# Performance work log

Measured on AMD Instinct MI355X. Metric: run time of the kernel, lower is better.

The kernel has to match this reference:

```python
import jax, jax.numpy as jnp
import numpy as np

D_MODEL = 256
POOL = 10  # Keras MaxPooling1D(pool_size=10) -> stride 10, padding 'same'


def setup_inputs() -> dict:
    key = jax.random.key(0)
    ks = jax.random.split(key, 11)
    B, S, D = 4, 4096, D_MODEL
    scale = 1.0 / np.sqrt(D)
    inp = {
        "v": jax.random.normal(ks[0], (B, S, D), jnp.float32),
        "k": jax.random.normal(ks[1], (B, S, D), jnp.float32),
        "q": jax.random.normal(ks[2], (B, S, D), jnp.float32),
        "wq": jax.random.normal(ks[3], (D, D), jnp.float32) * scale,
        "bq": jnp.zeros((D,), jnp.float32),
        "wk": jax.random.normal(ks[4], (D, D), jnp.float32) * scale,
        "bk": jnp.zeros((D,), jnp.float32),
        "wv": jax.random.normal(ks[5], (D, D), jnp.float32) * scale,
        "bv": jnp.zeros((D,), jnp.float32),
        "wo": jax.random.normal(ks[6], (D, D), jnp.float32) * scale,
        "bo": jnp.zeros((D,), jnp.float32),
    }
    return inp


def reference(v, k, q, wq, bq, wk, bk, wv, bv, wo, bo):
    d = q.shape[-1]
    qp = q @ wq + bq          # [B,Sq,D]
    kp = k @ wk + bk          # [B,Sk,D]
    vp = v @ wv + bv          # [B,Sk,D]
    scores = jnp.einsum('bqd,bkd->bqk', qp, kp) / jnp.sqrt(jnp.float32(d))
    # MaxPooling1D over the steps (Sq) axis, stride = pool_size, 'same' padding
    pooled = jax.lax.reduce_window(
        scores, -jnp.inf, jax.lax.max,
        window_dimensions=(1, POOL, 1),
        window_strides=(1, POOL, 1),
        padding='SAME')          # [B, ceil(Sq/10), Sk]
    attn = jax.nn.softmax(pooled, axis=-1)
    out = jnp.einsum('bqk,bkd->bqd', attn, vp)
    return out @ wo + bo
```

## Files before the change

### kernel.cpp

```cpp
#include <hip/hip_runtime.h>
#include <hip/hip_bf16.h>
#include <stdint.h>

typedef __attribute__((ext_vector_type(8))) short          bf16x8;
typedef __attribute__((ext_vector_type(4))) float          f32x4;
typedef __attribute__((ext_vector_type(4))) float          f4;
typedef __attribute__((ext_vector_type(8))) unsigned short u16x8;
typedef __attribute__((ext_vector_type(4))) unsigned short u16x4;

#define DEVINL __device__ __forceinline__

static constexpr int B  = 4;
static constexpr int S  = 4096;
static constexpr int D  = 256;
static constexpr int SP = 410;
static constexpr int KZ = 16;
static constexpr int MO = B * SP;
static constexpr size_t PSLICE = (size_t)MO * D;

DEVINL unsigned short f2bf(float x) {
  union { float f; unsigned u; } v; v.f = x;
  unsigned r = v.u + 0x7FFFu + ((v.u >> 16) & 1u);
  return (unsigned short)(r >> 16);
}

DEVINL f32x4 mfma16(bf16x8 a, bf16x8 b, f32x4 c) {
  return __builtin_amdgcn_mfma_f32_16x16x32_bf16(a, b, c, 0, 0, 0);
}

typedef const __attribute__((address_space(1))) void* gas_t;
typedef __attribute__((address_space(3))) void*       las_t;
DEVINL void gload16(const void* g, void* l) {
  __builtin_amdgcn_global_load_lds((gas_t)g, (las_t)l, 16, 0, 0);
}

DEVINL void cfence() { asm volatile("" ::: "memory"); }
DEVINL void barrier_mem() { cfence(); __builtin_amdgcn_s_barrier(); cfence(); }
DEVINL void lds_barrier() {
  asm volatile("s_waitcnt lgkmcnt(0)" ::: "memory");
  __builtin_amdgcn_s_barrier();
  cfence();
}
#define WAIT_VM(N) asm volatile("s_waitcnt vmcnt(" #N ")" ::: "memory")

__global__ __launch_bounds__(256) void cvtwt_kernel(
    const float* __restrict__ xq, const float* __restrict__ xk, const float* __restrict__ xv,
    const float* __restrict__ wq, const float* __restrict__ wk,
    const float* __restrict__ wv, const float* __restrict__ wo,
    unsigned short* __restrict__ oq, unsigned short* __restrict__ ok, unsigned short* __restrict__ ov,
    unsigned short* __restrict__ wt)
{
  int z = blockIdx.y;
  if (z == 3) {
    if (blockIdx.x >= 1024) return;
    int idx = blockIdx.x * 256 + threadIdx.x;
    int mat = idx >> 16;
    int r   = idx & 65535;
    int n   = r >> 8;
    int k   = r & 255;
    const float* w = (mat == 0) ? wq : (mat == 1) ? wk : (mat == 2) ? wv : wo;
    wt[idx] = f2bf(w[k * 256 + n]);
    return;
  }
  const float* x    = (z == 0) ? xq : (z == 1) ? xk : xv;
  unsigned short* o = (z == 0) ? oq : (z == 1) ? ok : ov;
  size_t i = ((size_t)blockIdx.x * 256 + threadIdx.x) * 8;
  f4 a = *reinterpret_cast<const f4*>(x + i);
  f4 c = *reinterpret_cast<const f4*>(x + i + 4);
  u16x8 h;
  h[0] = f2bf(a[0]); h[1] = f2bf(a[1]); h[2] = f2bf(a[2]); h[3] = f2bf(a[3]);
  h[4] = f2bf(c[0]); h[5] = f2bf(c[1]); h[6] = f2bf(c[2]); h[7] = f2bf(c[3]);
  *reinterpret_cast<u16x8*>(o + i) = h;
}

__global__ __launch_bounds__(512) void proj_kernel(
    const unsigned short* __restrict__ xq, const unsigned short* __restrict__ xk,
    const unsigned short* __restrict__ xv, const unsigned short* __restrict__ wt,
    const float* __restrict__ bq, const float* __restrict__ bk, const float* __restrict__ bv,
    unsigned short* __restrict__ qp, unsigned short* __restrict__ kp, unsigned short* __restrict__ vpT)
{
  int z = blockIdx.z;
  const unsigned short* X = (z == 0) ? xq : (z == 1) ? xk : xv;
  const unsigned short* W = wt + z * 65536;
  const float* bias       = (z == 0) ? bq : (z == 1) ? bk : bv;

  int m0 = blockIdx.x * 256;
  int n0 = blockIdx.y * 128;

  __shared__ __align__(16) struct { char A[2][32768]; char Bm[2][16384]; } sm;

  const char* Xc = (const char*)X;
  const char* Wc = (const char*)W;

  int tid  = threadIdx.x;
  int lane = tid & 63, wid = tid >> 6;
  int wr = wid >> 1, wc = wid & 1;
  int lrow = lane & 15, kseg = lane >> 4;

  f32x4 zero4 = {0.f, 0.f, 0.f, 0.f};
  f32x4 acc[4][4];
#pragma unroll
  for (int i = 0; i < 4; i++)
#pragma unroll
    for (int j = 0; j < 4; j++) acc[i][j] = zero4;

  auto stage = [&](int t, int buf) {
#pragma unroll
    for (int i = 0; i < 4; ++i) {
      int inst = wid * 4 + i;
      int sg   = inst * 64 + lane;
      int row  = sg >> 3, c16 = sg & 7;
      gload16(Xc + ((size_t)(m0 + row) << 9) + (t << 7) + ((c16 ^ (row & 7)) << 4),
              sm.A[buf] + inst * 1024);
    }
#pragma unroll
    for (int i = 0; i < 2; ++i) {
      int inst = wid * 2 + i;
      int sg   = inst * 64 + lane;
      int row  = sg >> 3, c16 = sg & 7;
      gload16(Wc + ((size_t)(n0 + row) << 9) + (t << 7) + ((c16 ^ (row & 7)) << 4),
              sm.Bm[buf] + inst * 1024);
    }
  };

  stage(0, 0);
#pragma unroll
  for (int t = 0; t < 4; ++t) {
    int cur = t & 1;
    if (t < 3) { stage(t + 1, cur ^ 1); WAIT_VM(6); } else { WAIT_VM(0); }
    barrier_mem();
    const char* Asm = sm.A[cur];
    const char* Bsm = sm.Bm[cur];
#pragma unroll
    for (int kk = 0; kk < 2; ++kk) {
      bf16x8 af[4], bfr[4];
#pragma unroll
      for (int mi = 0; mi < 4; ++mi) {
        int R = wr * 64 + mi * 16 + lrow;
        int c16 = (kk * 4 + kseg) ^ (R & 7);
        af[mi] = *reinterpret_cast<const bf16x8*>(Asm + R * 128 + c16 * 16);
      }
#pragma unroll
      for (int cf = 0; cf < 4; ++cf) {
        int nl = wc * 64 + cf * 16 + lrow;
        int c16 = (kk * 4 + kseg) ^ (nl & 7);
        bfr[cf] = *reinterpret_cast<const bf16x8*>(Bsm + nl * 128 + c16 * 16);
      }
#pragma unroll
      for (int mi = 0; mi < 4; ++mi)
#pragma unroll
        for (int cf = 0; cf < 4; ++cf)
          acc[mi][cf] = mfma16(af[mi], bfr[cf], acc[mi][cf]);
    }
    barrier_mem();
  }

  int r4 = kseg * 4;
  if (z < 2) {
    unsigned short* Out = (z == 0) ? qp : kp;
#pragma unroll
    for (int mi = 0; mi < 4; mi++)
#pragma unroll
      for (int cf = 0; cf < 4; cf++) {
        int n = n0 + wc * 64 + cf * 16 + lrow;
        float bv_ = bias[n];
#pragma unroll
        for (int r = 0; r < 4; r++) {
          int m = m0 + wr * 64 + mi * 16 + r4 + r;
          Out[(size_t)m * 256 + n] = f2bf(acc[mi][cf][r] + bv_);
        }
      }
  } else {
#pragma unroll
    for (int mi = 0; mi < 4; mi++)
#pragma unroll
      for (int cf = 0; cf < 4; cf++) {
        int n = n0 + wc * 64 + cf * 16 + lrow;
        float bv_ = bias[n];
        u16x4 hh;
#pragma unroll
        for (int r = 0; r < 4; r++) hh[r] = f2bf(acc[mi][cf][r] + bv_);
        int m  = m0 + wr * 64 + mi * 16 + r4;
        int bb = m >> 12, s = m & 4095;
        *reinterpret_cast<u16x4*>(&vpT[(size_t)bb * (256 * 4096) + (size_t)n * 4096 + s]) = hh;
      }
  }
}

__global__ __launch_bounds__(512) void scores_pool_kernel(
    const unsigned short* __restrict__ qp, const unsigned short* __restrict__ kp,
    float* __restrict__ pooled)
{
  int id   = blockIdx.x;
  int nb   = id & 31;
  int b    = (id >> 5) & 3;
  int half = id >> 7;
  int wb0  = half ? 9 : 0;
  int nwb  = half ? 8 : 9;
  int n0   = nb * 128;

  __shared__ __align__(16) struct { char A[2][32768]; char Bm[65536]; } sm;
  float* pm = (float*)sm.A[1];

  const char* qpc = (const char*)(qp + (size_t)b * S * 256);
  const char* kpc = (const char*)(kp + (size_t)b * S * 256);

  int tid  = threadIdx.x;
  int lane = tid & 63, wid = tid >> 6;
  int wr = wid >> 1, wc = wid & 1;
  int lrow = lane & 15, kseg = lane >> 4;
  int h = kseg;

#pragma unroll
  for (int i = 0; i < 8; ++i) {
    int inst = wid * 8 + i;
    int sg   = inst * 64 + lane;
    int row  = sg >> 5, c16 = sg & 31;
    gload16(kpc + ((size_t)(n0 + row) << 9) + (((size_t)(c16 ^ (row & 7))) << 4),
            sm.Bm + inst * 1024);
  }

  auto stageA = [&](int qbt, int ks, int buf) {
#pragma unroll
    for (int i = 0; i < 4; ++i) {
      int inst = wid * 4 + i;
      int sg   = inst * 64 + lane;
      int row  = sg >> 3, c16 = sg & 7;
      int q = qbt + row; q = (q < 0) ? 0 : ((q > S - 1) ? (S - 1) : q);
      gload16(qpc + ((size_t)q << 9) + (ks << 7) + ((c16 ^ (row & 7)) << 4),
              sm.A[buf] + inst * 1024);
    }
  };

  stageA(wb0 * 250 - 2, 0, 0);

  int gmax = nwb * 4;
  for (int i = 0; i < nwb; ++i) {
    int wb = wb0 + i, w0 = wb * 25;
    int qb = w0 * 10 - 2;
    int nwin = SP - w0; if (nwin > 25) nwin = 25;

    f32x4 zero4 = {0.f, 0.f, 0.f, 0.f};
    f32x4 acc[4][4];
#pragma unroll
    for (int mi = 0; mi < 4; mi++)
#pragma unroll
      for (int cf = 0; cf < 4; cf++) acc[mi][cf] = zero4;

#pragma unroll
    for (int ks = 0; ks < 4; ++ks) {
      int g  = (i << 2) | ks;
      int gn = g + 1;
      if (gn < gmax) {
        int i2 = gn >> 2, ks2 = gn & 3;
        stageA((wb0 + i2) * 250 - 2, ks2, gn & 1);
        WAIT_VM(4);
      } else {
        WAIT_VM(0);
      }
      barrier_mem();
      const char* Asm = sm.A[g & 1];
#pragma unroll
      for (int kk = 0; kk < 2; ++kk) {
        bf16x8 af[4], bfr[4];
#pragma unroll
        for (int mi = 0; mi < 4; ++mi) {
          int R = wr * 64 + mi * 16 + lrow;
          int c16 = (kk * 4 + kseg) ^ (R & 7);
          af[mi] = *reinterpret_cast<const bf16x8*>(Asm + R * 128 + c16 * 16);
        }
#pragma unroll
        for (int cf = 0; cf < 4; ++cf) {
          int nl = wc * 64 + cf * 16 + lrow;
          int c16 = ((ks << 3) + kk * 4 + kseg) ^ (nl & 7);
          bfr[cf] = *reinterpret_cast<const bf16x8*>(sm.Bm + nl * 512 + c16 * 16);
        }
#pragma unroll
        for (int mi = 0; mi < 4; ++mi)
#pragma unroll
          for (int cf = 0; cf < 4; ++cf)
            acc[mi][cf] = mfma16(af[mi], bfr[cf], acc[mi][cf]);
      }
      barrier_mem();
    }

#pragma unroll
    for (int c = 0; c < 2; ++c) {
      if (wc == c) {
#pragma unroll
        for (int mi = 0; mi < 4; ++mi) {
          int p = wr * 32 + mi * 8 + h * 2;
#pragma unroll
          for (int cf = 0; cf < 4; ++cf) {
            int col = cf * 16 + lrow;
            pm[p * 64 + col]       = fmaxf(acc[mi][cf][0], acc[mi][cf][1]);
            pm[(p + 1) * 64 + col] = fmaxf(acc[mi][cf][2], acc[mi][cf][3]);
          }
        }
      }
      lds_barrier();
      for (int s = tid; s < 1600; s += 512) {
        int j = s >> 6, col = s & 63;
        if (j < nwin) {
          float m = -3.4e38f;
#pragma unroll
          for (int t5 = 0; t5 < 5; ++t5) {
            int p  = 5 * j + t5;
            int q0 = qb + 2 * p;
            if (q0 >= 0 && q0 < S) m = fmaxf(m, pm[p * 64 + col]);
          }
          pooled[((size_t)b * SP + w0 + j) * 4096 + n0 + c * 64 + col] = m * 0.0625f;
        }
      }
      lds_barrier();
    }
  }
}

__global__ __launch_bounds__(256) void softmax_kernel(
    const float* __restrict__ pooled, unsigned short* __restrict__ attn)
{
  int row = blockIdx.x;
  const float* p = pooled + (size_t)row * 4096;
  unsigned short* a = attn + (size_t)row * 4096;
  int tid = threadIdx.x;
  int lane = tid & 63, wid = tid >> 6;

  f4 v[4];
  float mx = -3.4e38f;
#pragma unroll
  for (int i = 0; i < 4; i++) {
    v[i] = *reinterpret_cast<const f4*>(&p[i * 1024 + tid * 4]);
    mx = fmaxf(mx, fmaxf(fmaxf(v[i][0], v[i][1]), fmaxf(v[i][2], v[i][3])));
  }
#pragma unroll
  for (int off = 32; off > 0; off >>= 1) mx = fmaxf(mx, __shfl_xor(mx, off, 64));
  __shared__ float redm[4];
  __shared__ float reds[4];
  if (lane == 0) redm[wid] = mx;
  __syncthreads();
  mx = fmaxf(fmaxf(redm[0], redm[1]), fmaxf(redm[2], redm[3]));

  float e[16];
  float sum = 0.f;
#pragma unroll
  for (int i = 0; i < 4; i++)
#pragma unroll
    for (int j = 0; j < 4; j++) {
      float t = __expf(v[i][j] - mx);
      e[i * 4 + j] = t;
      sum += t;
    }
#pragma unroll
  for (int off = 32; off > 0; off >>= 1) sum += __shfl_xor(sum, off, 64);
  if (lane == 0) reds[wid] = sum;
  __syncthreads();
  sum = reds[0] + reds[1] + reds[2] + reds[3];
  float inv = 1.f / sum;
#pragma unroll
  for (int i = 0; i < 4; i++) {
    u16x4 o;
#pragma unroll
    for (int j = 0; j < 4; j++) o[j] = f2bf(e[i * 4 + j] * inv);
    *reinterpret_cast<u16x4*>(&a[i * 1024 + tid * 4]) = o;
  }
}

__global__ __launch_bounds__(256) void pv_kernel(
    const unsigned short* __restrict__ attn, const unsigned short* __restrict__ vpT,
    float* __restrict__ part)
{
  int bx = blockIdx.x;
  int b  = bx >> 2, mt = bx & 3;
  int m0 = mt * 128;
  int n0 = blockIdx.y * 128;
  int kz = blockIdx.z;
  int k0b = kz * 512;

  const char* Ac = (const char*)(attn + (size_t)b * SP * 4096);
  const char* Bc = (const char*)(vpT  + (size_t)b * 256 * 4096);
  float* Pz = part + (size_t)kz * PSLICE;

  __shared__ __align__(16) struct { char A[2][16384]; char Bm[2][16384]; } sm;

  int tid  = threadIdx.x;
  int lane = tid & 63, wid = tid >> 6;
  int wr = wid >> 1, wc = wid & 1;
  int lrow = lane & 15, kseg = lane >> 4;

  f32x4 zero4 = {0.f, 0.f, 0.f, 0.f};
  f32x4 acc[4][4];
#pragma unroll
  for (int i = 0; i < 4; i++)
#pragma unroll
    for (int j = 0; j < 4; j++) acc[i][j] = zero4;

  auto stage = [&](int t, int buf) {
#pragma unroll
    for (int i = 0; i < 4; ++i) {
      int inst = wid * 4 + i;
      int sg   = inst * 64 + lane;
      int row  = sg >> 3, c16 = sg & 7;
      int m = m0 + row; m = (m > SP - 1) ? (SP - 1) : m;
      gload16(Ac + (size_t)m * 8192 + k0b + (t << 7) + ((c16 ^ (row & 7)) << 4),
              sm.A[buf] + inst * 1024);
    }
#pragma unroll
    for (int i = 0; i < 4; ++i) {
      int inst = wid * 4 + i;
      int sg   = inst * 64 + lane;
      int row  = sg >> 3, c16 = sg & 7;
      gload16(Bc + (size_t)(n0 + row) * 8192 + k0b + (t << 7) + ((c16 ^ (row & 7)) << 4),
              sm.Bm[buf] + inst * 1024);
    }
  };

  stage(0, 0);
#pragma unroll
  for (int t = 0; t < 4; ++t) {
    int cur = t & 1;
    if (t < 3) { stage(t + 1, cur ^ 1); WAIT_VM(8); } else { WAIT_VM(0); }
    barrier_mem();
    const char* Asm = sm.A[cur];
    const char* Bsm = sm.Bm[cur];
#pragma unroll
    for (int kk = 0; kk < 2; ++kk) {
      bf16x8 af[4], bfr[4];
#pragma unroll
      for (int mi = 0; mi < 4; ++mi) {
        int R = wr * 64 + mi * 16 + lrow;
        int c16 = (kk * 4 + kseg) ^ (R & 7);
        af[mi] = *reinterpret_cast<const bf16x8*>(Asm + R * 128 + c16 * 16);
      }
#pragma unroll
      for (int cf = 0; cf < 4; ++cf) {
        int nl = wc * 64 + cf * 16 + lrow;
        int c16 = (kk * 4 + kseg) ^ (nl & 7);
        bfr[cf] = *reinterpret_cast<const bf16x8*>(Bsm + nl * 128 + c16 * 16);
      }
#pragma unroll
      for (int mi = 0; mi < 4; ++mi)
#pragma unroll
        for (int cf = 0; cf < 4; ++cf)
          acc[mi][cf] = mfma16(af[mi], bfr[cf], acc[mi][cf]);
    }
    barrier_mem();
  }

  int r4 = kseg * 4;
#pragma unroll
  for (int mi = 0; mi < 4; mi++)
#pragma unroll
    for (int cf = 0; cf < 4; cf++) {
      int n = n0 + wc * 64 + cf * 16 + lrow;
#pragma unroll
      for (int r = 0; r < 4; r++) {
        int m = m0 + wr * 64 + mi * 16 + r4 + r;
        if (m < SP) Pz[((size_t)b * SP + m) * 256 + n] = acc[mi][cf][r];
      }
    }
}

__global__ __launch_bounds__(256) void reduce_kernel(
    const float* __restrict__ part, unsigned short* __restrict__ ctxb)
{
  size_t i = (size_t)blockIdx.x * 256 + threadIdx.x;
  float s = 0.f;
#pragma unroll
  for (int z = 0; z < KZ; ++z) s += part[z * PSLICE + i];
  ctxb[i] = f2bf(s);
}

__global__ __launch_bounds__(512) void out_kernel(
    const unsigned short* __restrict__ ctxb, const unsigned short* __restrict__ woT,
    const float* __restrict__ bo, float* __restrict__ out)
{
  int m0 = blockIdx.x * 256;
  int n0 = blockIdx.y * 128;

  __shared__ __align__(16) struct { char A[2][32768]; char Bm[2][16384]; } sm;

  const char* Xc = (const char*)ctxb;
  const char* Wc = (const char*)woT;

  int tid  = threadIdx.x;
  int lane = tid & 63, wid = tid >> 6;
  int wr = wid >> 1, wc = wid & 1;
  int lrow = lane & 15, kseg = lane >> 4;

  f32x4 zero4 = {0.f, 0.f, 0.f, 0.f};
  f32x4 acc[4][4];
#pragma unroll
  for (int i = 0; i < 4; i++)
#pragma unroll
    for (int j = 0; j < 4; j++) acc[i][j] = zero4;

  auto stage = [&](int t, int buf) {
#pragma unroll
    for (int i = 0; i < 4; ++i) {
      int inst = wid * 4 + i;
      int sg   = inst * 64 + lane;
      int row  = sg >> 3, c16 = sg & 7;
      int m = m0 + row; m = (m > MO - 1) ? (MO - 1) : m;
      gload16(Xc + ((size_t)m << 9) + (t << 7) + ((c16 ^ (row & 7)) << 4),
              sm.A[buf] + inst * 1024);
    }
#pragma unroll
    for (int i = 0; i < 2; ++i) {
      int inst = wid * 2 + i;
      int sg   = inst * 64 + lane;
      int row  = sg >> 3, c16 = sg & 7;
      gload16(Wc + ((size_t)(n0 + row) << 9) + (t << 7) + ((c16 ^ (row & 7)) << 4),
              sm.Bm[buf] + inst * 1024);
    }
  };

  stage(0, 0);
#pragma unroll
  for (int t = 0; t < 4; ++t) {
    int cur = t & 1;
    if (t < 3) { stage(t + 1, cur ^ 1); WAIT_VM(6); } else { WAIT_VM(0); }
    barrier_mem();
    const char* Asm = sm.A[cur];
    const char* Bsm = sm.Bm[cur];
#pragma unroll
    for (int kk = 0; kk < 2; ++kk) {
      bf16x8 af[4], bfr[4];
#pragma unroll
      for (int mi = 0; mi < 4; ++mi) {
        int R = wr * 64 + mi * 16 + lrow;
        int c16 = (kk * 4 + kseg) ^ (R & 7);
        af[mi] = *reinterpret_cast<const bf16x8*>(Asm + R * 128 + c16 * 16);
      }
#pragma unroll
      for (int cf = 0; cf < 4; ++cf) {
        int nl = wc * 64 + cf * 16 + lrow;
        int c16 = (kk * 4 + kseg) ^ (nl & 7);
        bfr[cf] = *reinterpret_cast<const bf16x8*>(Bsm + nl * 128 + c16 * 16);
      }
#pragma unroll
      for (int mi = 0; mi < 4; ++mi)
#pragma unroll
        for (int cf = 0; cf < 4; ++cf)
          acc[mi][cf] = mfma16(af[mi], bfr[cf], acc[mi][cf]);
    }
    barrier_mem();
  }

  int r4 = kseg * 4;
#pragma unroll
  for (int mi = 0; mi < 4; mi++)
#pragma unroll
    for (int cf = 0; cf < 4; cf++) {
      int n = n0 + wc * 64 + cf * 16 + lrow;
      float bv_ = bo[n];
#pragma unroll
      for (int r = 0; r < 4; r++) {
        int m = m0 + wr * 64 + mi * 16 + r4 + r;
        if (m < MO) out[(size_t)m * 256 + n] = acc[mi][cf][r] + bv_;
      }
    }
}

extern "C" void kernel_launch(void* const* d_in, const int* in_sizes, int n_in,
                              void* d_out, int out_size, void* d_ws, size_t ws_size,
                              hipStream_t stream)
{
  const float* v  = (const float*)d_in[0];
  const float* k  = (const float*)d_in[1];
  const float* q  = (const float*)d_in[2];
  const float* wq = (const float*)d_in[3];
  const float* bq = (const float*)d_in[4];
  const float* wk = (const float*)d_in[5];
  const float* bk = (const float*)d_in[6];
  const float* wv = (const float*)d_in[7];
  const float* bv = (const float*)d_in[8];
  const float* wo = (const float*)d_in[9];
  const float* bo = (const float*)d_in[10];
  float* out = (float*)d_out;

  char* ws = (char*)d_ws;
  size_t off = 0;
  auto alloc = [&](size_t bytes) -> void* {
    void* p = ws + off;
    off += (bytes + 255) & ~(size_t)255;
    return p;
  };
  unsigned short* qp   = (unsigned short*)alloc((size_t)B * S * D * 2);
  unsigned short* kp   = (unsigned short*)alloc((size_t)B * S * D * 2);
  unsigned short* vpT  = (unsigned short*)alloc((size_t)B * S * D * 2);
  unsigned short* wt   = (unsigned short*)alloc((size_t)4 * 256 * 256 * 2);
  unsigned short* ctxb = (unsigned short*)alloc(PSLICE * 2);
  char* shared_region  = (char*)alloc((size_t)B * SP * 4096 * 4);
  unsigned short* attn = (unsigned short*)alloc((size_t)B * SP * 4096 * 2);

  unsigned short* qx = (unsigned short*)shared_region;
  unsigned short* kx = qx + (size_t)B * S * D;
  unsigned short* vx = kx + (size_t)B * S * D;
  float* pooled = (float*)shared_region;
  float* part   = (float*)shared_region;

  cvtwt_kernel<<<dim3(2048, 4), 256, 0, stream>>>(q, k, v, wq, wk, wv, wo, qx, kx, vx, wt);
  proj_kernel<<<dim3(64, 2, 3), 512, 0, stream>>>(qx, kx, vx, wt, bq, bk, bv, qp, kp, vpT);
  scores_pool_kernel<<<256, 512, 0, stream>>>(qp, kp, pooled);
  softmax_kernel<<<B * SP, 256, 0, stream>>>(pooled, attn);
  pv_kernel<<<dim3(16, 2, KZ), 256, 0, stream>>>(attn, vpT, part);
  reduce_kernel<<<(int)(PSLICE / 256), 256, 0, stream>>>(part, ctxb);
  out_kernel<<<dim3(7, 2), 512, 0, stream>>>(ctxb, wt + 3 * 65536, bo, out);
}
```

Baseline: 221.9 us.

## Load Q fragments directly into registers with double-buffered prefetch, drop LDS A staging

The scores kernel no longer stages Q tiles through double-buffered LDS with per-k-step barriers. Each wave now loads its A fragments straight from global memory into registers, prefetching the next k-slice (and the next window block) while MFMAs run, and raises wave priority around the MFMA block. The pooling scratch buffer gets its own padded LDS region (stride 68) to reduce bank conflicts. This removes eight barriers per window and the LDS round trip for A, at the cost of uncoalesced 16-byte global loads, possibly redundant across waves, and more VGPR pressure.

```diff
diff --git a/kernel.cpp b/kernel.cpp
--- a/kernel.cpp
+++ b/kernel.cpp
@@ -199,8 +199,9 @@
   int nwb  = half ? 8 : 9;
   int n0   = nb * 128;
 
-  __shared__ __align__(16) struct { char A[2][32768]; char Bm[65536]; } sm;
-  float* pm = (float*)sm.A[1];
+  __shared__ __align__(16) struct { char Bm[65536]; float pm[128 * 68]; } sm;
+  char* Bsm = sm.Bm;
+  float* pm = sm.pm;
 
   const char* qpc = (const char*)(qp + (size_t)b * S * 256);
   const char* kpc = (const char*)(kp + (size_t)b * S * 256);
@@ -217,72 +218,69 @@
     int sg   = inst * 64 + lane;
     int row  = sg >> 5, c16 = sg & 31;
     gload16(kpc + ((size_t)(n0 + row) << 9) + (((size_t)(c16 ^ (row & 7))) << 4),
-            sm.Bm + inst * 1024);
-  }
-
-  auto stageA = [&](int qbt, int ks, int buf) {
-#pragma unroll
-    for (int i = 0; i < 4; ++i) {
-      int inst = wid * 4 + i;
-      int sg   = inst * 64 + lane;
-      int row  = sg >> 3, c16 = sg & 7;
-      int q = qbt + row; q = (q < 0) ? 0 : ((q > S - 1) ? (S - 1) : q);
-      gload16(qpc + ((size_t)q << 9) + (ks << 7) + ((c16 ^ (row & 7)) << 4),
-              sm.A[buf] + inst * 1024);
+            Bsm + inst * 1024);
+  }
+  WAIT_VM(0);
+  barrier_mem();
+
+  const char* abase[4];
+  auto setbase = [&](int qb) {
+#pragma unroll
+    for (int mi = 0; mi < 4; ++mi) {
+      int q = qb + wr * 64 + mi * 16 + lrow;
+      q = (q < 0) ? 0 : ((q > S - 1) ? (S - 1) : q);
+      abase[mi] = qpc + ((size_t)q << 9) + kseg * 16;
     }
   };
-
-  stageA(wb0 * 250 - 2, 0, 0);
-
-  int gmax = nwb * 4;
+  auto loada = [&](bf16x8* dst, int ksoff) {
+#pragma unroll
+    for (int mi = 0; mi < 4; ++mi)
+#pragma unroll
+      for (int kk = 0; kk < 2; ++kk)
+        dst[mi * 2 + kk] = *reinterpret_cast<const bf16x8*>(abase[mi] + ksoff + kk * 64);
+  };
+
+  f32x4 acc[4][4];
+  auto mma_step = [&](int ks, const bf16x8* ause) {
+    __builtin_amdgcn_s_setprio(1);
+#pragma unroll
+    for (int kk = 0; kk < 2; ++kk) {
+      bf16x8 bfr[4];
+#pragma unroll
+      for (int cf = 0; cf < 4; ++cf) {
+        int nl = wc * 64 + cf * 16 + lrow;
+        int c16 = ((ks << 3) + (kk << 2) + kseg) ^ (nl & 7);
+        bfr[cf] = *reinterpret_cast<const bf16x8*>(Bsm + nl * 512 + c16 * 16);
+      }
+#pragma unroll
+      for (int mi = 0; mi < 4; ++mi)
+#pragma unroll
+        for (int cf = 0; cf < 4; ++cf)
+          acc[mi][cf] = mfma16(ause[mi * 2 + kk], bfr[cf], acc[mi][cf]);
+    }
+    __builtin_amdgcn_s_setprio(0);
+  };
+
+  bf16x8 aA[8], aB[8];
+  setbase(wb0 * 250 - 2);
+  loada(aA, 0);
+
   for (int i = 0; i < nwb; ++i) {
     int wb = wb0 + i, w0 = wb * 25;
     int qb = w0 * 10 - 2;
     int nwin = SP - w0; if (nwin > 25) nwin = 25;
 
     f32x4 zero4 = {0.f, 0.f, 0.f, 0.f};
-    f32x4 acc[4][4];
 #pragma unroll
     for (int mi = 0; mi < 4; mi++)
 #pragma unroll
       for (int cf = 0; cf < 4; cf++) acc[mi][cf] = zero4;
 
-#pragma unroll
-    for (int ks = 0; ks < 4; ++ks) {
-      int g  = (i << 2) | ks;
-      int gn = g + 1;
-      if (gn < gmax) {
-        int i2 = gn >> 2, ks2 = gn & 3;
-        stageA((wb0 + i2) * 250 - 2, ks2, gn & 1);
-        WAIT_VM(4);
-      } else {
-        WAIT_VM(0);
-      }
-      barrier_mem();
-      const char* Asm = sm.A[g & 1];
-#pragma unroll
-      for (int kk = 0; kk < 2; ++kk) {
-        bf16x8 af[4], bfr[4];
-#pragma unroll
-        for (int mi = 0; mi < 4; ++mi) {
-          int R = wr * 64 + mi * 16 + lrow;
-          int c16 = (kk * 4 + kseg) ^ (R & 7);
-          af[mi] = *reinterpret_cast<const bf16x8*>(Asm + R * 128 + c16 * 16);
-        }
-#pragma unroll
-        for (int cf = 0; cf < 4; ++cf) {
-          int nl = wc * 64 + cf * 16 + lrow;
-          int c16 = ((ks << 3) + kk * 4 + kseg) ^ (nl & 7);
-          bfr[cf] = *reinterpret_cast<const bf16x8*>(sm.Bm + nl * 512 + c16 * 16);
-        }
-#pragma unroll
-        for (int mi = 0; mi < 4; ++mi)
-#pragma unroll
-          for (int cf = 0; cf < 4; ++cf)
-            acc[mi][cf] = mfma16(af[mi], bfr[cf], acc[mi][cf]);
-      }
-      barrier_mem();
-    }
+    loada(aB, 128);  mma_step(0, aA);
+    loada(aA, 256);  mma_step(1, aB);
+    loada(aB, 384);  mma_step(2, aA);
+    if (i + 1 < nwb) { setbase(qb + 250);  loada(aA, 0); }
+    mma_step(3, aB);
 
 #pragma unroll
     for (int c = 0; c < 2; ++c) {
@@ -293,8 +291,8 @@
 #pragma unroll
           for (int cf = 0; cf < 4; ++cf) {
             int col = cf * 16 + lrow;
-            pm[p * 64 + col]       = fmaxf(acc[mi][cf][0], acc[mi][cf][1]);
-            pm[(p + 1) * 64 + col] = fmaxf(acc[mi][cf][2], acc[mi][cf][3]);
+            pm[p * 68 + col]       = fmaxf(acc[mi][cf][0], acc[mi][cf][1]);
+            pm[(p + 1) * 68 + col] = fmaxf(acc[mi][cf][2], acc[mi][cf][3]);
           }
         }
       }
@@ -307,7 +305,7 @@
           for (int t5 = 0; t5 < 5; ++t5) {
             int p  = 5 * j + t5;
             int q0 = qb + 2 * p;
-            if (q0 >= 0 && q0 < S) m = fmaxf(m, pm[p * 64 + col]);
+            if (q0 >= 0 && q0 < S) m = fmaxf(m, pm[p * 68 + col]);
           }
           pooled[((size_t)b * SP + w0 + j) * 4096 + n0 + c * 64 + col] = m * 0.0625f;
         }
```

New measurement: 256.6 us. 15.7% more time.
